# Kernel optimization log

Measured on AMD Instinct MI355X. Metric: run time of the kernel, lower is better.

## Reference

```python
import jax, jax.numpy as jnp
import numpy as np

NUM_CLASSES = 20  # support_labels drawn from [0, 20); torch.unique over 200 samples yields all 20 w.h.p.


def setup_inputs() -> dict:
    key = jax.random.key(0)
    k1, k2, k3 = jax.random.split(key, 3)
    support_features = jax.random.normal(k1, (8, 200, 512), dtype=jnp.float32)
    support_labels = jax.random.randint(k2, (200,), 0, NUM_CLASSES, dtype=jnp.int64)
    query_features = jax.random.normal(k3, (8, 1024, 512), dtype=jnp.float32)
    return {
        "support_features": support_features,
        "support_labels": support_labels,
        "query_features": query_features,
    }


def _task_cov(x):
    # x: (P, T, F) -> per-phi covariance over the T samples, factor 1/(T-1)
    T = x.shape[1]
    xc = x - jnp.mean(x, axis=1, keepdims=True)
    return jnp.einsum("ptf,ptg->pfg", xc, xc) / (T - 1)


def reference(support_features, support_labels, query_features):
    P, T, F = support_features.shape
    C = NUM_CLASSES

    onehot = jax.nn.one_hot(support_labels, C, dtype=support_features.dtype)  # (T, C)
    counts = onehot.sum(axis=0)                                               # (C,)
    counts_safe = jnp.maximum(counts, 1.0)

    # per-class means: (P, C, F)
    class_means = jnp.einsum("ptf,tc->pcf", support_features, onehot) / counts_safe[None, :, None]

    # per-class covariance with 1/(n_c - 1) factor (matches _estimate_cov after transpose)
    centered = support_features[:, :, None, :] - class_means[:, None, :, :]   # (P, T, C, F)
    masked = centered * onehot[None, :, :, None]                               # zero out other classes
    denom = jnp.maximum(counts - 1.0, 1.0)
    class_cov = jnp.einsum("ptcf,ptcg->pcfg", masked, masked) / denom[None, :, None, None]

    task_cov = _task_cov(support_features)                                     # (P, F, F)

    lam = counts_safe / (counts_safe + 1.0)                                    # (C,)
    eye = jnp.eye(F, dtype=support_features.dtype)
    cov_reg = (lam[None, :, None, None] * class_cov
               + (1.0 - lam)[None, :, None, None] * task_cov[:, None]
               + eye)                                                          # (P, C, F, F)
    precision = jnp.linalg.inv(cov_reg)                                        # (P, C, F, F)

    # Mahalanobis quadratic form: diff^T P diff for every (phi, query, class)
    diff = class_means[:, None, :, :] - query_features[:, :, None, :]          # (P, Q, C, F)
    quad = jnp.einsum("pqcf,pcfg,pqcg->pqc", diff, precision, diff)
    mean_logits = (-quad).mean(axis=0)                                         # (Q, C)
    return mean_logits, class_means
```

## Files before the change

kernel.cpp:

```cpp
#include <hip/hip_runtime.h>

#define P 8
#define T 200
#define C 20
#define F 512
#define NQ 1024
#define MAXN 40
#define MMAX (T + MAXN)
#define PACK ((MMAX*(MMAX+1))/2)
#define PACKA 29280
#define PACKT 40960
#define QL (NQ*C)
#define NB 16
#define NTF 512
#define ETH 72
#define XQS 72

#define NBLK_FACTOR 160
#define NBLK_SQ     128
#define NBLK_MEANS  160
#define NBLK_QNORM  128
#define NBLK_TOTAL  (NBLK_FACTOR + NBLK_SQ + NBLK_MEANS + NBLK_QNORM)

enum : int {
  OFF_G    = 0,
  OFF_SQ   = OFF_G   + P*T*T,
  OFF_G1   = OFF_SQ  + P*T*NQ,
  OFF_GG   = OFF_G1  + P*T,
  OFF_GM   = OFF_GG  + P,
  OFF_GMC  = OFF_GM  + P*T*C,
  OFF_MM   = OFF_GMC + P*C,
  OFF_GQ   = OFF_MM  + P*C,
  OFF_QN   = OFF_GQ  + P*NQ,
  OFF_MQ   = OFF_QN  + P*NQ,
  OFF_W    = OFF_MQ  + P*C*NQ,
  OFF_QUAD = OFF_W   + P*C*PACKT,
  OFF_CLSF = OFF_QUAD+ P*NQ*C,
  OFF_INT  = OFF_CLSF+ C*8
};

typedef _Float16 f16x8 __attribute__((ext_vector_type(8)));
typedef _Float16 f16x4 __attribute__((ext_vector_type(4)));
typedef _Float16 f16x2 __attribute__((ext_vector_type(2)));
typedef float    f32x4 __attribute__((ext_vector_type(4)));

__device__ __forceinline__ int offr(int i){ return (i*(i+1))>>1; }

__device__ __forceinline__ int rowS(int i){
  int a = i >> 2, r = i & 3;
  return 8*a*(a+1) + 4*r*(a+1);
}

__device__ __forceinline__ int rowT(int r){
  const int R = r >> 6, s = r & 63;
  const int base = 4096 * ((R*(R+1)) >> 1);
  return base + s*((R+1) << 6);
}

__device__ __forceinline__ int row_of(int e){
  int i = (int)((sqrtf(8.f*(float)e + 1.f) - 1.f) * 0.5f);
  while (offr(i+1) <= e) ++i;
  while (offr(i) > e) --i;
  return i;
}

__device__ __forceinline__ int row_ofS(int e){
  int i = (int)sqrtf(2.f*(float)e);
  if (i > MMAX-1) i = MMAX-1;
  while (i < MMAX-1 && rowS(i+1) <= e) ++i;
  while (i > 0 && rowS(i) > e) --i;
  return i;
}

__global__ void k_setup(const int* lab, float* ws){
  int c = threadIdx.x;
  if (c >= C) return;
  int* wsI = (int*)(ws + OFF_INT);
  int n = 0;
  for (int t = 0; t < T; ++t){
    if (lab[t] == c){ if (n < MAXN) wsI[C + c*MAXN + n] = t; ++n; }
  }
  if (n > MAXN) n = MAXN;
  wsI[c] = n;
  float nf    = (float)n;
  float nsafe = fmaxf(nf, 1.0f);
  float dn    = fmaxf(nf - 1.0f, 1.0f);
  float lam   = nsafe / (nsafe + 1.0f);
  float sv    = (1.0f - lam) / (float)(T - 1);
  float av    = lam / dn;
  float* cf = ws + OFF_CLSF + c*8;
  cf[0] = nsafe; cf[1] = dn; cf[2] = lam; cf[3] = sv; cf[4] = av;
  cf[5] = sqrtf(sv); cf[6] = sqrtf(av); cf[7] = 0.0f;
}

__global__ __launch_bounds__(512) void k_gram(const float* __restrict__ X,
                                              float* __restrict__ ws){
  __shared__ _Float16 RH[64*XQS], RL[64*XQS];
  __shared__ _Float16 CH[256*XQS], CL[256*XQS];
  const int p = blockIdx.y, t0 = blockIdx.x*64;
  const int tid = threadIdx.x;
  const float* Xp = X + (size_t)p*T*F;
  const int wv = tid >> 6, ln = tid & 63;
  const int lr = ln & 15, lg = ln >> 4;
  const int wt = (wv & 1) * 32;
  const int wq = (wv >> 1) * 64;

  f32x4 acc[2][4] = {};

  for (int kb = 0; kb < F; kb += 64){
    for (int e = tid; e < 64*16; e += 512){
      const int r = e >> 4, l4 = (e & 15) * 4;
      float4 v = (t0 + r < T) ? *(const float4*)&Xp[(size_t)(t0+r)*F + kb + l4]
                              : make_float4(0.f,0.f,0.f,0.f);
      _Float16 h0=(_Float16)v.x, h1=(_Float16)v.y, h2=(_Float16)v.z, h3=(_Float16)v.w;
      f16x4 hv = {h0,h1,h2,h3};
      f16x4 lv = {(_Float16)(v.x-(float)h0),(_Float16)(v.y-(float)h1),
                  (_Float16)(v.z-(float)h2),(_Float16)(v.w-(float)h3)};
      *(f16x4*)&RH[r*XQS + l4] = hv;
      *(f16x4*)&RL[r*XQS + l4] = lv;
    }
    for (int e = tid; e < 256*16; e += 512){
      const int r = e >> 4, l4 = (e & 15) * 4;
      float4 v = (r < T) ? *(const float4*)&Xp[(size_t)r*F + kb + l4]
                         : make_float4(0.f,0.f,0.f,0.f);
      _Float16 h0=(_Float16)v.x, h1=(_Float16)v.y, h2=(_Float16)v.z, h3=(_Float16)v.w;
      f16x4 hv = {h0,h1,h2,h3};
      f16x4 lv = {(_Float16)(v.x-(float)h0),(_Float16)(v.y-(float)h1),
                  (_Float16)(v.z-(float)h2),(_Float16)(v.w-(float)h3)};
      *(f16x4*)&CH[r*XQS + l4] = hv;
      *(f16x4*)&CL[r*XQS + l4] = lv;
    }
    __syncthreads();
    #pragma unroll
    for (int s = 0; s < 2; ++s){
      const int ko = s*32 + 8*lg;
      f16x8 bh[4], bl[4];
      #pragma unroll
      for (int j = 0; j < 4; ++j){
        const int qr = wq + j*16 + lr;
        bh[j] = *(const f16x8*)&CH[qr*XQS + ko];
        bl[j] = *(const f16x8*)&CL[qr*XQS + ko];
      }
      #pragma unroll
      for (int i = 0; i < 2; ++i){
        const int tr = wt + i*16 + lr;
        f16x8 ah = *(const f16x8*)&RH[tr*XQS + ko];
        f16x8 al = *(const f16x8*)&RL[tr*XQS + ko];
        #pragma unroll
        for (int j = 0; j < 4; ++j){
          acc[i][j] = __builtin_amdgcn_mfma_f32_16x16x32_f16(ah, bh[j], acc[i][j], 0, 0, 0);
          acc[i][j] = __builtin_amdgcn_mfma_f32_16x16x32_f16(ah, bl[j], acc[i][j], 0, 0, 0);
          acc[i][j] = __builtin_amdgcn_mfma_f32_16x16x32_f16(al, bh[j], acc[i][j], 0, 0, 0);
        }
      }
    }
    __syncthreads();
  }
  float* Gp = ws + OFF_G + (size_t)p*T*T;
  #pragma unroll
  for (int i = 0; i < 2; ++i){
    const int tb = t0 + wt + i*16 + lg*4;
    #pragma unroll
    for (int j = 0; j < 4; ++j){
      const int col = wq + j*16 + lr;
      if (col < T){
        #pragma unroll
        for (int r = 0; r < 4; ++r){
          const int t = tb + r;
          if (t < T) Gp[t*T + col] = acc[i][j][r];
        }
      }
    }
  }
}

__global__ __launch_bounds__(256) void k_pstats_a(float* ws){
  const int p = blockIdx.y, bx = blockIdx.x;
  const int w = threadIdx.x >> 6, lane = threadIdx.x & 63;
  const int* wsI = (const int*)(ws + OFF_INT);
  const float* Gp = ws + OFF_G + (size_t)p*T*T;
  float* g1 = ws + OFF_G1 + p*T;
  float* Gm = ws + OFF_GM + (size_t)p*T*C;
  for (int rr = 0; rr < 2; ++rr){
    const int t = bx*8 + w*2 + rr;
    float s = 0.f;
    for (int u = lane; u < T; u += 64) s += Gp[t*T + u];
    for (int off = 32; off; off >>= 1) s += __shfl_down(s, off, 64);
    if (lane == 0) g1[t] = s * (1.0f/T);
    if (lane < C){
      int c = lane, nn = wsI[c];
      const int* idxc = wsI + C + c*MAXN;
      float sc = 0.f;
      for (int j = 0; j < nn; ++j) sc += Gp[t*T + idxc[j]];
      Gm[t*C + c] = sc / ws[OFF_CLSF + c*8];
    }
  }
}

__global__ __launch_bounds__(256) void k_pstats_b(float* ws){
  __shared__ float red[64];
  const int p = blockIdx.x, tid = threadIdx.x;
  const int* wsI = (const int*)(ws + OFF_INT);
  const float* g1 = ws + OFF_G1 + p*T;
  const float* Gm = ws + OFF_GM + (size_t)p*T*C;
  if (tid < 64){
    float s = 0.f;
    for (int t = tid; t < T; t += 64) s += g1[t];
    red[tid] = s;
  }
  __syncthreads();
  if (tid == 0){
    float s = 0.f;
    for (int k = 0; k < 64; ++k) s += red[k];
    ws[OFF_GG + p] = s * (1.0f/T);
  }
  if (tid < C){
    int c = tid, nn = wsI[c];
    const int* idxc = wsI + C + c*MAXN;
    float s = 0.f;
    for (int t = 0; t < T; ++t) s += Gm[t*C + c];
    ws[OFF_GMC + p*C + c] = s * (1.0f/T);
    float s2 = 0.f;
    for (int j = 0; j < nn; ++j) s2 += Gm[idxc[j]*C + c];
    ws[OFF_MM + p*C + c] = s2 / ws[OFF_CLSF + c*8];
  }
}

__global__ __launch_bounds__(256) void k_qstats(float* ws){
  __shared__ float red[4][64];
  const int p = blockIdx.y;
  const int qb = blockIdx.x*64;
  const int chunk = threadIdx.x >> 6, lane = threadIdx.x & 63;
  const int q = qb + lane;
  const int* wsI = (const int*)(ws + OFF_INT);
  const float* SQp = ws + OFF_SQ + (size_t)p*T*NQ;
  float s = 0.f;
  for (int t = chunk*50; t < chunk*50 + 50; ++t) s += SQp[t*NQ + q];
  red[chunk][lane] = s;
  __syncthreads();
  if (chunk == 0){
    float tot = red[0][lane] + red[1][lane] + red[2][lane] + red[3][lane];
    ws[OFF_GQ + p*NQ + q] = tot * (1.0f/T);
  }
  for (int c = chunk; c < C; c += 4){
    int nn = wsI[c];
    const int* idxc = wsI + C + c*MAXN;
    float sc = 0.f;
    for (int j = 0; j < nn; ++j) sc += SQp[idxc[j]*NQ + q];
    ws[OFF_MQ + ((size_t)(p*C + c))*NQ + q] = sc / ws[OFF_CLSF + c*8];
  }
}


union __align__(16) BigShared {
  struct { float Lp[PACKA]; float Sb[16*228]; float Dv[NB][NB+1]; } f;
  struct { _Float16 XHs[64*XQS], XLs[64*XQS], QHs[256*XQS], QLs[256*XQS]; } q;
};

__global__ __launch_bounds__(NTF) void k_big(const float* __restrict__ X,
                                             const float* __restrict__ Qf,
                                             float* __restrict__ ws,
                                             float* __restrict__ out){
  __shared__ BigShared u;
  const int bid = blockIdx.x;
  const int tid = threadIdx.x;
  const int* wsI = (const int*)(ws + OFF_INT);

  if (bid < NBLK_FACTOR){
    float* Lp = u.f.Lp;
    float* Sb = u.f.Sb;
    float (&Dv)[NB][NB+1] = u.f.Dv;
    const int blk = bid, p = blk / C, c = blk % C;
    const int n = wsI[c];
    const int m = T + n;
    const int* idxc = wsI + C + c*MAXN;
    const float* cf = ws + OFF_CLSF + c*8;
    const float sv = cf[3], av = cf[4], sqsa = cf[5]*cf[6];
    const float* Gp  = ws + OFF_G  + (size_t)p*T*T;
    const float* g1p = ws + OFF_G1 + p*T;
    const float  ggv = ws[OFF_GG + p];
    const float* Gmp = ws + OFF_GM + (size_t)p*T*C;
    const float gmcv = ws[OFF_GMC + p*C + c];
    const float mmv  = ws[OFF_MM  + p*C + c];

    for (int e = tid; e < PACKA; e += NTF){
      int i = row_ofS(e);
      int j = e - rowS(i);
      float v = 0.f;
      if (i < m && j <= i){
        if (i < T){
          v = sv*(Gp[i*T + j] - g1p[i] - g1p[j] + ggv);
          if (j == i) v += 1.0f;
        } else {
          int ua = idxc[i - T];
          if (j < T){
            v = sqsa*(Gp[ua*T + j] - Gmp[j*C + c] - g1p[ua] + gmcv);
          } else {
            int ub = idxc[j - T];
            v = av*(Gp[ua*T + ub] - Gmp[ua*C + c] - Gmp[ub*C + c] + mmv);
            if (j == i) v += 1.0f;
          }
        }
      }
      Lp[e] = v;
    }
    __syncthreads();

    for (int k0 = 0; k0 < m; k0 += NB){
      if (tid < 64){
        const int lane = tid;
        float a[NB];
        #pragma unroll
        for (int j = 0; j < NB; ++j){
          a[j] = 0.f;
          if (lane < NB && j <= lane) a[j] = Lp[rowS(k0+lane) + k0 + j];
        }
        #pragma unroll
        for (int k = 0; k < NB; ++k){
          float akk = __shfl(a[k], k, 64);
          float inv = rsqrtf(akk);
          a[k] *= inv;
          #pragma unroll
          for (int j = k+1; j < NB; ++j){
            float ljk = __shfl(a[k], j, 64);
            a[j] -= a[k] * ljk;
          }
        }
        float x[NB];
        #pragma unroll
        for (int i = 0; i < NB; ++i){
          float Lii = __shfl(a[i], i, 64);
          float sxx = 0.f;
          #pragma unroll
          for (int k2 = 0; k2 < i; ++k2){
            float Lik = __shfl(a[k2], i, 64);
            sxx += Lik * x[k2];
          }
          float tt = ((i == lane) ? 1.f : 0.f) - sxx;
          x[i] = tt / Lii;
        }
        if (lane < NB){
          #pragma unroll
          for (int i = 0; i < NB; ++i){
            Dv[i][lane] = (i >= lane) ? x[i] : 0.f;
            if (i >= lane) Lp[rowS(k0+i) + k0 + lane] = x[i];
          }
        }
      }
      __syncthreads();

      for (int r = k0 + NB + tid; r < m; r += NTF){
        const int o = rowS(r) + k0;
        float4 A0 = *(const float4*)&Lp[o];
        float4 A1 = *(const float4*)&Lp[o+4];
        float4 A2 = *(const float4*)&Lp[o+8];
        float4 A3 = *(const float4*)&Lp[o+12];
        float ar[NB] = {A0.x,A0.y,A0.z,A0.w, A1.x,A1.y,A1.z,A1.w,
                        A2.x,A2.y,A2.z,A2.w, A3.x,A3.y,A3.z,A3.w};
        float sr[NB];
        #pragma unroll
        for (int j = 0; j < NB; ++j){
          float s = 0.f;
          #pragma unroll
          for (int kk = 0; kk <= j; ++kk) s += ar[kk] * Dv[j][kk];
          sr[j] = s;
        }
        *(float4*)&Lp[o]    = make_float4(sr[0], sr[1], sr[2], sr[3]);
        *(float4*)&Lp[o+4]  = make_float4(sr[4], sr[5], sr[6], sr[7]);
        *(float4*)&Lp[o+8]  = make_float4(sr[8], sr[9], sr[10], sr[11]);
        *(float4*)&Lp[o+12] = make_float4(sr[12], sr[13], sr[14], sr[15]);
      }
      __syncthreads();

      const int rs = m - k0 - NB;
      if (rs > 0){
        const int base = k0 + NB;
        const int nt4 = (rs + 3) >> 2;
        const int ntile = (nt4*(nt4+1)) >> 1;
        for (int e2 = tid; e2 < ntile; e2 += NTF){
          const int ti = row_of(e2);
          const int tj = e2 - offr(ti);
          const int gi0 = base + 4*ti, gj0 = base + 4*tj;
          const float* pa0 = &Lp[rowS(gi0)   + k0];
          const float* pa1 = &Lp[rowS(gi0+1) + k0];
          const float* pa2 = &Lp[rowS(gi0+2) + k0];
          const float* pa3 = &Lp[rowS(gi0+3) + k0];
          const float* pb0 = &Lp[rowS(gj0)   + k0];
          const float* pb1 = &Lp[rowS(gj0+1) + k0];
          const float* pb2 = &Lp[rowS(gj0+2) + k0];
          const float* pb3 = &Lp[rowS(gj0+3) + k0];
          float acc[4][4] = {};
          #pragma unroll
          for (int kk = 0; kk < NB; kk += 4){
            float4 a0 = *(const float4*)(pa0+kk);
            float4 a1 = *(const float4*)(pa1+kk);
            float4 a2 = *(const float4*)(pa2+kk);
            float4 a3 = *(const float4*)(pa3+kk);
            float4 b0 = *(const float4*)(pb0+kk);
            float4 b1 = *(const float4*)(pb1+kk);
            float4 b2 = *(const float4*)(pb2+kk);
            float4 b3 = *(const float4*)(pb3+kk);
            acc[0][0] += a0.x*b0.x + a0.y*b0.y + a0.z*b0.z + a0.w*b0.w;
            acc[0][1] += a0.x*b1.x + a0.y*b1.y + a0.z*b1.z + a0.w*b1.w;
            acc[0][2] += a0.x*b2.x + a0.y*b2.y + a0.z*b2.z + a0.w*b2.w;
            acc[0][3] += a0.x*b3.x + a0.y*b3.y + a0.z*b3.z + a0.w*b3.w;
            acc[1][0] += a1.x*b0.x + a1.y*b0.y + a1.z*b0.z + a1.w*b0.w;
            acc[1][1] += a1.x*b1.x + a1.y*b1.y + a1.z*b1.z + a1.w*b1.w;
            acc[1][2] += a1.x*b2.x + a1.y*b2.y + a1.z*b2.z + a1.w*b2.w;
            acc[1][3] += a1.x*b3.x + a1.y*b3.y + a1.z*b3.z + a1.w*b3.w;
            acc[2][0] += a2.x*b0.x + a2.y*b0.y + a2.z*b0.z + a2.w*b0.w;
            acc[2][1] += a2.x*b1.x + a2.y*b1.y + a2.z*b1.z + a2.w*b1.w;
            acc[2][2] += a2.x*b2.x + a2.y*b2.y + a2.z*b2.z + a2.w*b2.w;
            acc[2][3] += a2.x*b3.x + a2.y*b3.y + a2.z*b3.z + a2.w*b3.w;
            acc[3][0] += a3.x*b0.x + a3.y*b0.y + a3.z*b0.z + a3.w*b0.w;
            acc[3][1] += a3.x*b1.x + a3.y*b1.y + a3.z*b1.z + a3.w*b1.w;
            acc[3][2] += a3.x*b2.x + a3.y*b2.y + a3.z*b2.z + a3.w*b2.w;
            acc[3][3] += a3.x*b3.x + a3.y*b3.y + a3.z*b3.z + a3.w*b3.w;
          }
          #pragma unroll
          for (int u2 = 0; u2 < 4; ++u2){
            const int gi = gi0 + u2;
            if (gi < m){
              const int og = rowS(gi);
              if (gj0 + 3 <= gi){
                float4 t = *(float4*)&Lp[og + gj0];
                t.x -= acc[u2][0]; t.y -= acc[u2][1]; t.z -= acc[u2][2]; t.w -= acc[u2][3];
                *(float4*)&Lp[og + gj0] = t;
              } else {
                #pragma unroll
                for (int v = 0; v < 4; ++v){
                  const int gj = gj0 + v;
                  if (gj <= gi) Lp[og + gj] -= acc[u2][v];
                }
              }
            }
          }
        }
      }
      __syncthreads();
    }

    for (int I = 1; I < MMAX/NB; ++I){
      const int i0 = I*NB;
      if (i0 >= m) break;
      const int nct = i0 >> 2;
      const int rt = tid & 3, ct = tid >> 2;
      const int rt4 = rt*4;
      const int j0 = ct*4;
      int o0 = 0, o1 = 0, o2 = 0, o3 = 0;
      if (tid < 4*nct){
        const int r0 = i0 + rt4;
        o0 = rowS(r0); o1 = rowS(r0+1); o2 = rowS(r0+2); o3 = rowS(r0+3);
        float acc[4][4] = {};
        for (int k = j0; k < i0; k += 4){
          float4 l0 = *(const float4*)&Lp[o0+k];
          float4 l1 = *(const float4*)&Lp[o1+k];
          float4 l2 = *(const float4*)&Lp[o2+k];
          float4 l3 = *(const float4*)&Lp[o3+k];
          float4 x0 = *(const float4*)&Lp[rowS(k)  +j0];
          float4 x1 = *(const float4*)&Lp[rowS(k+1)+j0];
          float4 x2 = *(const float4*)&Lp[rowS(k+2)+j0];
          float4 x3 = *(const float4*)&Lp[rowS(k+3)+j0];
          acc[0][0] += l0.x*x0.x + l0.y*x1.x + l0.z*x2.x + l0.w*x3.x;
          acc[0][1] += l0.x*x0.y + l0.y*x1.y + l0.z*x2.y + l0.w*x3.y;
          acc[0][2] += l0.x*x0.z + l0.y*x1.z + l0.z*x2.z + l0.w*x3.z;
          acc[0][3] += l0.x*x0.w + l0.y*x1.w + l0.z*x2.w + l0.w*x3.w;
          acc[1][0] += l1.x*x0.x + l1.y*x1.x + l1.z*x2.x + l1.w*x3.x;
          acc[1][1] += l1.x*x0.y + l1.y*x1.y + l1.z*x2.y + l1.w*x3.y;
          acc[1][2] += l1.x*x0.z + l1.y*x1.z + l1.z*x2.z + l1.w*x3.z;
          acc[1][3] += l1.x*x0.w + l1.y*x1.w + l1.z*x2.w + l1.w*x3.w;
          acc[2][0] += l2.x*x0.x + l2.y*x1.x + l2.z*x2.x + l2.w*x3.x;
          acc[2][1] += l2.x*x0.y + l2.y*x1.y + l2.z*x2.y + l2.w*x3.y;
          acc[2][2] += l2.x*x0.z + l2.y*x1.z + l2.z*x2.z + l2.w*x3.z;
          acc[2][3] += l2.x*x0.w + l2.y*x1.w + l2.z*x2.w + l2.w*x3.w;
          acc[3][0] += l3.x*x0.x + l3.y*x1.x + l3.z*x2.x + l3.w*x3.x;
          acc[3][1] += l3.x*x0.y + l3.y*x1.y + l3.z*x2.y + l3.w*x3.y;
          acc[3][2] += l3.x*x0.z + l3.y*x1.z + l3.z*x2.z + l3.w*x3.z;
          acc[3][3] += l3.x*x0.w + l3.y*x1.w + l3.z*x2.w + l3.w*x3.w;
        }
        *(float4*)&Sb[(rt4  )*228 + j0] = make_float4(acc[0][0], acc[0][1], acc[0][2], acc[0][3]);
        *(float4*)&Sb[(rt4+1)*228 + j0] = make_float4(acc[1][0], acc[1][1], acc[1][2], acc[1][3]);
        *(float4*)&Sb[(rt4+2)*228 + j0] = make_float4(acc[2][0], acc[2][1], acc[2][2], acc[2][3]);
        *(float4*)&Sb[(rt4+3)*228 + j0] = make_float4(acc[3][0], acc[3][1], acc[3][2], acc[3][3]);
      }
      __syncthreads();
      if (tid < 4*nct){
        float acc[4][4] = {};
        for (int s = 0; s < rt4 + 4; ++s){
          const float d0 = Lp[o0 + i0 + s];
          const float d1 = Lp[o1 + i0 + s];
          const float d2 = Lp[o2 + i0 + s];
          const float d3 = Lp[o3 + i0 + s];
          const float4 sv4 = *(const float4*)&Sb[s*228 + j0];
          acc[0][0] += d0*sv4.x; acc[0][1] += d0*sv4.y; acc[0][2] += d0*sv4.z; acc[0][3] += d0*sv4.w;
          acc[1][0] += d1*sv4.x; acc[1][1] += d1*sv4.y; acc[1][2] += d1*sv4.z; acc[1][3] += d1*sv4.w;
          acc[2][0] += d2*sv4.x; acc[2][1] += d2*sv4.y; acc[2][2] += d2*sv4.z; acc[2][3] += d2*sv4.w;
          acc[3][0] += d3*sv4.x; acc[3][1] += d3*sv4.y; acc[3][2] += d3*sv4.z; acc[3][3] += d3*sv4.w;
        }
        *(float4*)&Lp[o0 + j0] = make_float4(-acc[0][0], -acc[0][1], -acc[0][2], -acc[0][3]);
        *(float4*)&Lp[o1 + j0] = make_float4(-acc[1][0], -acc[1][1], -acc[1][2], -acc[1][3]);
        *(float4*)&Lp[o2 + j0] = make_float4(-acc[2][0], -acc[2][1], -acc[2][2], -acc[2][3]);
        *(float4*)&Lp[o3 + j0] = make_float4(-acc[3][0], -acc[3][1], -acc[3][2], -acc[3][3]);
      }
      __syncthreads();
    }

    _Float16* WH = (_Float16*)(ws + OFF_W) + (size_t)blk * (2*PACKT);
    _Float16* WL = WH + PACKT;
    for (int e = tid; e < 64*64; e += NTF){
      int s = e >> 6, j = e & 63, r = s;
      float v = (r < m && j <= r) ? Lp[rowS(r) + j] : 0.f;
      _Float16 h = (_Float16)v;
      WH[e] = h; WL[e] = (_Float16)(v - (float)h);
    }
    for (int e = tid; e < 64*128; e += NTF){
      int s = e >> 7, j = e & 127, r = 64 + s;
      float v = (r < m && j <= r) ? Lp[rowS(r) + j] : 0.f;
      _Float16 h = (_Float16)v;
      WH[4096 + e] = h; WL[4096 + e] = (_Float16)(v - (float)h);
    }
    for (int e = tid; e < 64*192; e += NTF){
      int x = e >> 6;
      int s = (x*171) >> 9;
      int j = e - s*192, r = 128 + s;
      float v = (r < m && j <= r) ? Lp[rowS(r) + j] : 0.f;
      _Float16 h = (_Float16)v;
      WH[12288 + e] = h; WL[12288 + e] = (_Float16)(v - (float)h);
    }
    for (int e = tid; e < 64*256; e += NTF){
      int s = e >> 8, j = e & 255, r = 192 + s;
      float v = (r < m && j <= r) ? Lp[rowS(r) + j] : 0.f;
      _Float16 h = (_Float16)v;
      WH[24576 + e] = h; WL[24576 + e] = (_Float16)(v - (float)h);
    }

  } else if (bid < NBLK_FACTOR + NBLK_SQ){
    const int sb = bid - NBLK_FACTOR;
    const int p = sb >> 4, rem = sb & 15;
    const int t0 = (rem >> 2) * 64;
    const int qb = (rem & 3) * 256;
    _Float16* XH = u.q.XHs; _Float16* XL = u.q.XLs;
    _Float16* QH = u.q.QHs; _Float16* Qlo = u.q.QLs;
    const float* Xp = X  + (size_t)p*T*F;
    const float* Qp = Qf + (size_t)p*NQ*F;
    const int wv = tid >> 6, ln = tid & 63;
    const int lr = ln & 15, lg = ln >> 4;
    const int wt = (wv & 1) * 32;
    const int wq = (wv >> 1) * 64;

    f32x4 acc[2][4] = {};

    for (int kb = 0; kb < F; kb += 64){
      for (int e = tid; e < 64*16; e += NTF){
        const int r = e >> 4, l4 = (e & 15) * 4;
        float4 v = (t0 + r < T) ? *(const float4*)&Xp[(size_t)(t0+r)*F + kb + l4]
                                : make_float4(0.f,0.f,0.f,0.f);
        _Float16 h0=(_Float16)v.x, h1=(_Float16)v.y, h2=(_Float16)v.z, h3=(_Float16)v.w;
        f16x4 hv = {h0,h1,h2,h3};
        f16x4 lv = {(_Float16)(v.x-(float)h0),(_Float16)(v.y-(float)h1),
                    (_Float16)(v.z-(float)h2),(_Float16)(v.w-(float)h3)};
        *(f16x4*)&XH[r*XQS + l4] = hv;
        *(f16x4*)&XL[r*XQS + l4] = lv;
      }
      for (int e = tid; e < 256*16; e += NTF){
        const int r = e >> 4, l4 = (e & 15) * 4;
        float4 v = *(const float4*)&Qp[(size_t)(qb+r)*F + kb + l4];
        _Float16 h0=(_Float16)v.x, h1=(_Float16)v.y, h2=(_Float16)v.z, h3=(_Float16)v.w;
        f16x4 hv = {h0,h1,h2,h3};
        f16x4 lv = {(_Float16)(v.x-(float)h0),(_Float16)(v.y-(float)h1),
                    (_Float16)(v.z-(float)h2),(_Float16)(v.w-(float)h3)};
        *(f16x4*)&QH[r*XQS + l4] = hv;
        *(f16x4*)&Qlo[r*XQS + l4] = lv;
      }
      __syncthreads();
      #pragma unroll
      for (int s = 0; s < 2; ++s){
        const int ko = s*32 + 8*lg;
        f16x8 bh[4], bl[4];
        #pragma unroll
        for (int j = 0; j < 4; ++j){
          const int qr = wq + j*16 + lr;
          bh[j] = *(const f16x8*)&QH[qr*XQS + ko];
          bl[j] = *(const f16x8*)&Qlo[qr*XQS + ko];
        }
        #pragma unroll
        for (int i = 0; i < 2; ++i){
          const int tr = wt + i*16 + lr;
          f16x8 ah = *(const f16x8*)&XH[tr*XQS + ko];
          f16x8 al = *(const f16x8*)&XL[tr*XQS + ko];
          #pragma unroll
          for (int j = 0; j < 4; ++j){
            acc[i][j] = __builtin_amdgcn_mfma_f32_16x16x32_f16(ah, bh[j], acc[i][j], 0, 0, 0);
            acc[i][j] = __builtin_amdgcn_mfma_f32_16x16x32_f16(ah, bl[j], acc[i][j], 0, 0, 0);
            acc[i][j] = __builtin_amdgcn_mfma_f32_16x16x32_f16(al, bh[j], acc[i][j], 0, 0, 0);
          }
        }
      }
      __syncthreads();
    }
    float* SQp = ws + OFF_SQ + (size_t)p*T*NQ;
    #pragma unroll
    for (int i = 0; i < 2; ++i){
      const int tb = t0 + wt + i*16 + lg*4;
      #pragma unroll
      for (int j = 0; j < 4; ++j){
        const int qc = qb + wq + j*16 + lr;
        #pragma unroll
        for (int r = 0; r < 4; ++r){
          const int t = tb + r;
          if (t < T) SQp[t*NQ + qc] = acc[i][j][r];
        }
      }
    }

  } else if (bid < NBLK_FACTOR + NBLK_SQ + NBLK_MEANS){
    const int mb = bid - NBLK_FACTOR - NBLK_SQ;
    const int p = mb / C, c = mb % C;
    const int n = wsI[c];
    const int* idxc = wsI + C + c*MAXN;
    const float nf = ws[OFF_CLSF + c*8];
    const float* Xp = X + (size_t)p*T*F;
    float* o = out + QL + (size_t)(p*C + c)*F;
    for (int f = tid; f < F; f += NTF){
      float s = 0.f;
      for (int j = 0; j < n; ++j) s += Xp[idxc[j]*F + f];
      o[f] = s / nf;
    }

  } else {
    const int qb2 = bid - NBLK_FACTOR - NBLK_SQ - NBLK_MEANS;
    const int w = tid >> 6, lane = tid & 63;
    const int row0 = qb2*64 + w*8;
    for (int i = 0; i < 8; ++i){
      const int row = row0 + i;
      const float4* q4p = (const float4*)(Qf + (size_t)row*F);
      float4 v0 = q4p[lane];
      float4 v1 = q4p[lane + 64];
      float s = v0.x*v0.x + v0.y*v0.y + v0.z*v0.z + v0.w*v0.w
              + v1.x*v1.x + v1.y*v1.y + v1.z*v1.z + v1.w*v1.w;
      for (int off = 32; off; off >>= 1) s += __shfl_down(s, off, 64);
      if (lane == 0) ws[OFF_QN + row] = s;
    }
  }
}

__global__ __launch_bounds__(256) void k_apply(float* ws){
  __shared__ __align__(16) _Float16 EtH[64*ETH];
  __shared__ __align__(16) _Float16 EtL[64*ETH];
  __shared__ float Ef[32*65];
  __shared__ float Part[4][64];
  const int p = blockIdx.z, c = blockIdx.y, q0 = blockIdx.x*64;
  const int tid = threadIdx.x;
  const int* wsI = (const int*)(ws + OFF_INT);
  const int n = wsI[c], m = T + n;
  const int* idxc = wsI + C + c*MAXN;
  const float* cf = ws + OFF_CLSF + c*8;
  const float sqs = cf[5], sqa = cf[6];
  const float gmcv = ws[OFF_GMC + p*C + c];
  const float mmv  = ws[OFF_MM  + p*C + c];
  const float* Gmp = ws + OFF_GM + (size_t)p*T*C;
  const float* SQp = ws + OFF_SQ + (size_t)p*T*NQ;
  const float* gqp = ws + OFF_GQ + p*NQ + q0;
  const float* qnp = ws + OFF_QN + p*NQ + q0;
  const float* mqp = ws + OFF_MQ + ((size_t)(p*C + c))*NQ + q0;

  const int wv = tid >> 6, ln = tid & 63;
  const int lr = ln & 15;
  const int lg = ln >> 4;
  const _Float16* WH = (const _Float16*)(ws + OFF_W) + (size_t)(p*C + c)*(2*PACKT);
  const _Float16* WL = WH + PACKT;
  int aoff[4];
  #pragma unroll
  for (int i = 0; i < 4; ++i){
    const int t = wv + 4*i;
    aoff[i] = rowT(16*t + lr) + 8*lg;
  }

  f32x4 acc[4][4] = {};

  for (int h = 0; h < 4; ++h){
    for (int ch = 0; ch < 2; ++ch){
      const int jbl = ch*32;
      const int jb = h*64 + jbl;
      for (int e = tid; e < 32*64; e += 256){
        const int jl = e >> 6, q = e & 63;
        const int j = jb + jl;
        float v = 0.f;
        if (j < T){
          v = sqs*(Gmp[j*C + c] - SQp[j*NQ + q0 + q] - gmcv + gqp[q]);
        } else if (j < m){
          const int u2 = idxc[j - T];
          v = sqa*(Gmp[u2*C + c] - SQp[u2*NQ + q0 + q] - mmv + mqp[q]);
        }
        Ef[jl*65 + q] = v;
      }
      __syncthreads();
      for (int e = tid; e < 16*64; e += 256){
        const int jp = e & 15, q = e >> 4;
        const int jl = 2*jp;
        const float v0 = Ef[jl*65 + q];
        const float v1 = Ef[(jl+1)*65 + q];
        const _Float16 h0 = (_Float16)v0, h1 = (_Float16)v1;
        f16x2 hv; hv[0] = h0; hv[1] = h1;
        f16x2 lv; lv[0] = (_Float16)(v0 - (float)h0); lv[1] = (_Float16)(v1 - (float)h1);
        *(f16x2*)&EtH[q*ETH + jbl + jl] = hv;
        *(f16x2*)&EtL[q*ETH + jbl + jl] = lv;
      }
      __syncthreads();
    }

    #pragma unroll
    for (int sl = 0; sl < 2; ++sl){
      const int s = 2*h + sl;
      if (2*s > wv + 12) continue;
      const int k0 = 32*s;
      const int bo = lr*ETH + (k0 - 64*h) + 8*lg;
      f16x8 bh[4], bl[4];
      #pragma unroll
      for (int ct2 = 0; ct2 < 4; ++ct2){
        bh[ct2] = *(const f16x8*)&EtH[ct2*16*ETH + bo];
        bl[ct2] = *(const f16x8*)&EtL[ct2*16*ETH + bo];
      }
      #pragma unroll
      for (int i = 0; i < 4; ++i){
        const int t = wv + 4*i;
        if (2*s <= t){
          f16x8 ah = *(const f16x8*)(WH + aoff[i] + k0);
          f16x8 al = *(const f16x8*)(WL + aoff[i] + k0);
          #pragma unroll
          for (int ct2 = 0; ct2 < 4; ++ct2){
            acc[i][ct2] = __builtin_amdgcn_mfma_f32_16x16x32_f16(ah, bh[ct2], acc[i][ct2], 0, 0, 0);
            acc[i][ct2] = __builtin_amdgcn_mfma_f32_16x16x32_f16(ah, bl[ct2], acc[i][ct2], 0, 0, 0);
            acc[i][ct2] = __builtin_amdgcn_mfma_f32_16x16x32_f16(al, bh[ct2], acc[i][ct2], 0, 0, 0);
          }
        }
      }
    }
  }

  #pragma unroll
  for (int ct2 = 0; ct2 < 4; ++ct2){
    float sthread = 0.f;
    #pragma unroll
    for (int i = 0; i < 4; ++i){
      const f32x4 a4 = acc[i][ct2];
      sthread += a4[0]*a4[0] + a4[1]*a4[1] + a4[2]*a4[2] + a4[3]*a4[3];
    }
    sthread += __shfl_xor(sthread, 16, 64);
    sthread += __shfl_xor(sthread, 32, 64);
    if (ln < 16) Part[wv][ct2*16 + ln] = sthread;
  }
  __syncthreads();
  if (tid < 64){
    const float tt = Part[0][tid] + Part[1][tid] + Part[2][tid] + Part[3][tid];
    const float quad = mmv - 2.f*mqp[tid] + qnp[tid] - tt;
    ws[OFF_QUAD + ((size_t)p*NQ + q0 + tid)*C + c] = quad;
  }
}

__global__ void k_logits(const float* ws, float* out){
  int lin = blockIdx.x*256 + threadIdx.x;
  if (lin < QL){
    float s = 0.f;
    for (int p = 0; p < P; ++p) s += ws[OFF_QUAD + (size_t)p*NQ*C + lin];
    out[lin] = -s * (1.0f/P);
  }
}

extern "C" void kernel_launch(void* const* d_in, const int* in_sizes, int n_in,
                              void* d_out, int out_size, void* d_ws, size_t ws_size,
                              hipStream_t stream){
  const float* X   = (const float*)d_in[0];
  const int*   lab = (const int*)d_in[1];
  const float* Qf  = (const float*)d_in[2];
  float* out = (float*)d_out;
  float* ws  = (float*)d_ws;

  k_setup   <<<1, 64, 0, stream>>>(lab, ws);
  k_gram    <<<dim3(4,P), 512, 0, stream>>>(X, ws);
  k_pstats_a<<<dim3(25,P), 256, 0, stream>>>(ws);
  k_pstats_b<<<P, 256, 0, stream>>>(ws);
  k_big     <<<NBLK_TOTAL, NTF, 0, stream>>>(X, Qf, ws, out);
  k_qstats  <<<dim3(16,P), 256, 0, stream>>>(ws);
  k_apply   <<<dim3(16,C,P), 256, 0, stream>>>(ws);
  k_logits  <<<QL/256, 256, 0, stream>>>(ws, out);
}
```

Baseline: 538.3 us.

## Fuse pstats_a into gram, qstats into apply, logits via atomics

```diff
diff --git a/kernel.cpp b/kernel.cpp
--- a/kernel.cpp
+++ b/kernel.cpp
@@ -72,8 +72,10 @@
   return i;
 }
 
-__global__ void k_setup(const int* lab, float* ws){
-  int c = threadIdx.x;
+__global__ void k_setup(const int* lab, float* ws, float* out){
+  const int tid = threadIdx.x;
+  for (int i = tid; i < QL; i += 256) out[i] = 0.f;
+  int c = tid;
   if (c >= C) return;
   int* wsI = (int*)(ws + OFF_INT);
   int n = 0;
@@ -172,27 +174,28 @@
       }
     }
   }
-}
-
-__global__ __launch_bounds__(256) void k_pstats_a(float* ws){
-  const int p = blockIdx.y, bx = blockIdx.x;
-  const int w = threadIdx.x >> 6, lane = threadIdx.x & 63;
-  const int* wsI = (const int*)(ws + OFF_INT);
-  const float* Gp = ws + OFF_G + (size_t)p*T*T;
-  float* g1 = ws + OFF_G1 + p*T;
-  float* Gm = ws + OFF_GM + (size_t)p*T*C;
-  for (int rr = 0; rr < 2; ++rr){
-    const int t = bx*8 + w*2 + rr;
-    float s = 0.f;
-    for (int u = lane; u < T; u += 64) s += Gp[t*T + u];
-    for (int off = 32; off; off >>= 1) s += __shfl_down(s, off, 64);
-    if (lane == 0) g1[t] = s * (1.0f/T);
-    if (lane < C){
-      int c = lane, nn = wsI[c];
-      const int* idxc = wsI + C + c*MAXN;
-      float sc = 0.f;
-      for (int j = 0; j < nn; ++j) sc += Gp[t*T + idxc[j]];
-      Gm[t*C + c] = sc / ws[OFF_CLSF + c*8];
+  __syncthreads();
+
+  {
+    const int* wsI = (const int*)(ws + OFF_INT);
+    float* g1 = ws + OFF_G1 + p*T;
+    float* Gm = ws + OFF_GM + (size_t)p*T*C;
+    const int w = tid >> 6, lane = tid & 63;
+    for (int rr = 0; rr < 8; ++rr){
+      const int t = t0 + w*8 + rr;
+      if (t < T){
+        float s = 0.f;
+        for (int u2 = lane; u2 < T; u2 += 64) s += Gp[t*T + u2];
+        for (int off = 32; off; off >>= 1) s += __shfl_down(s, off, 64);
+        if (lane == 0) g1[t] = s * (1.0f/T);
+        if (lane < C){
+          int c = lane, nn = wsI[c];
+          const int* idxc = wsI + C + c*MAXN;
+          float sc = 0.f;
+          for (int j = 0; j < nn; ++j) sc += Gp[t*T + idxc[j]];
+          Gm[t*C + c] = sc / ws[OFF_CLSF + c*8];
+        }
+      }
     }
   }
 }
@@ -223,31 +226,6 @@
     float s2 = 0.f;
     for (int j = 0; j < nn; ++j) s2 += Gm[idxc[j]*C + c];
     ws[OFF_MM + p*C + c] = s2 / ws[OFF_CLSF + c*8];
-  }
-}
-
-__global__ __launch_bounds__(256) void k_qstats(float* ws){
-  __shared__ float red[4][64];
-  const int p = blockIdx.y;
-  const int qb = blockIdx.x*64;
-  const int chunk = threadIdx.x >> 6, lane = threadIdx.x & 63;
-  const int q = qb + lane;
-  const int* wsI = (const int*)(ws + OFF_INT);
-  const float* SQp = ws + OFF_SQ + (size_t)p*T*NQ;
-  float s = 0.f;
-  for (int t = chunk*50; t < chunk*50 + 50; ++t) s += SQp[t*NQ + q];
-  red[chunk][lane] = s;
-  __syncthreads();
-  if (chunk == 0){
-    float tot = red[0][lane] + red[1][lane] + red[2][lane] + red[3][lane];
-    ws[OFF_GQ + p*NQ + q] = tot * (1.0f/T);
-  }
-  for (int c = chunk; c < C; c += 4){
-    int nn = wsI[c];
-    const int* idxc = wsI + C + c*MAXN;
-    float sc = 0.f;
-    for (int j = 0; j < nn; ++j) sc += SQp[idxc[j]*NQ + q];
-    ws[OFF_MQ + ((size_t)(p*C + c))*NQ + q] = sc / ws[OFF_CLSF + c*8];
   }
 }
 
@@ -644,11 +622,13 @@
   }
 }
 
-__global__ __launch_bounds__(256) void k_apply(float* ws){
+__global__ __launch_bounds__(256) void k_apply(float* ws, float* out){
   __shared__ __align__(16) _Float16 EtH[64*ETH];
   __shared__ __align__(16) _Float16 EtL[64*ETH];
   __shared__ float Ef[32*65];
   __shared__ float Part[4][64];
+  __shared__ float redq[4][64];
+  __shared__ float gql[64], mql[64];
   const int p = blockIdx.z, c = blockIdx.y, q0 = blockIdx.x*64;
   const int tid = threadIdx.x;
   const int* wsI = (const int*)(ws + OFF_INT);
@@ -660,9 +640,25 @@
   const float mmv  = ws[OFF_MM  + p*C + c];
   const float* Gmp = ws + OFF_GM + (size_t)p*T*C;
   const float* SQp = ws + OFF_SQ + (size_t)p*T*NQ;
-  const float* gqp = ws + OFF_GQ + p*NQ + q0;
   const float* qnp = ws + OFF_QN + p*NQ + q0;
-  const float* mqp = ws + OFF_MQ + ((size_t)(p*C + c))*NQ + q0;
+
+  {
+    const int chunk = tid >> 6, lq = tid & 63;
+    float s = 0.f;
+    for (int t = chunk*50; t < chunk*50 + 50; ++t) s += SQp[t*NQ + q0 + lq];
+    redq[chunk][lq] = s;
+    float s2 = 0.f;
+    for (int j = chunk; j < n; j += 4) s2 += SQp[idxc[j]*NQ + q0 + lq];
+    __syncthreads();
+    if (chunk == 0)
+      gql[lq] = (redq[0][lq] + redq[1][lq] + redq[2][lq] + redq[3][lq]) * (1.0f/T);
+    __syncthreads();
+    redq[chunk][lq] = s2;
+    __syncthreads();
+    if (chunk == 0)
+      mql[lq] = (redq[0][lq] + redq[1][lq] + redq[2][lq] + redq[3][lq]) / cf[0];
+    __syncthreads();
+  }
 
   const int wv = tid >> 6, ln = tid & 63;
   const int lr = ln & 15;
@@ -687,10 +683,10 @@
         const int j = jb + jl;
         float v = 0.f;
         if (j < T){
-          v = sqs*(Gmp[j*C + c] - SQp[j*NQ + q0 + q] - gmcv + gqp[q]);
+          v = sqs*(Gmp[j*C + c] - SQp[j*NQ + q0 + q] - gmcv + gql[q]);
         } else if (j < m){
           const int u2 = idxc[j - T];
-          v = sqa*(Gmp[u2*C + c] - SQp[u2*NQ + q0 + q] - mmv + mqp[q]);
+          v = sqa*(Gmp[u2*C + c] - SQp[u2*NQ + q0 + q] - mmv + mql[q]);
         }
         Ef[jl*65 + q] = v;
       }
@@ -753,17 +749,8 @@
   __syncthreads();
   if (tid < 64){
     const float tt = Part[0][tid] + Part[1][tid] + Part[2][tid] + Part[3][tid];
-    const float quad = mmv - 2.f*mqp[tid] + qnp[tid] - tt;
-    ws[OFF_QUAD + ((size_t)p*NQ + q0 + tid)*C + c] = quad;
-  }
-}
-
-__global__ void k_logits(const float* ws, float* out){
-  int lin = blockIdx.x*256 + threadIdx.x;
-  if (lin < QL){
-    float s = 0.f;
-    for (int p = 0; p < P; ++p) s += ws[OFF_QUAD + (size_t)p*NQ*C + lin];
-    out[lin] = -s * (1.0f/P);
+    const float quad = mmv - 2.f*mql[tid] + qnp[tid] - tt;
+    atomicAdd(&out[(size_t)(q0 + tid)*C + c], -quad * (1.0f/P));
   }
 }
 
@@ -776,12 +763,9 @@
   float* out = (float*)d_out;
   float* ws  = (float*)d_ws;
 
-  k_setup   <<<1, 64, 0, stream>>>(lab, ws);
+  k_setup   <<<1, 256, 0, stream>>>(lab, ws, out);
   k_gram    <<<dim3(4,P), 512, 0, stream>>>(X, ws);
-  k_pstats_a<<<dim3(25,P), 256, 0, stream>>>(ws);
   k_pstats_b<<<P, 256, 0, stream>>>(ws);
   k_big     <<<NBLK_TOTAL, NTF, 0, stream>>>(X, Qf, ws, out);
-  k_qstats  <<<dim3(16,P), 256, 0, stream>>>(ws);
-  k_apply   <<<dim3(16,C,P), 256, 0, stream>>>(ws);
-  k_logits  <<<QL/256, 256, 0, stream>>>(ws, out);
-}
+  k_apply   <<<dim3(16,C,P), 256, 0, stream>>>(ws, out);
+}
```

After: 555.9 us. 1.03x slower.
